# Performance work log

Measured on AMD Instinct MI355X. Metric: run time of the kernel, lower is better.

The kernel has to match this reference:

```python
import jax, jax.numpy as jnp
import numpy as np

N_NODES = 100000
N_EDGES = 800000
IN_DIM = 7
HID = 64
HEADS1 = 4
NUM_CLUSTERS = 4
NEG_SLOPE = 0.2


def setup_inputs() -> dict:
    key = jax.random.key(0)
    ks = jax.random.split(key, 24)
    s = 0.1
    inp = {
        "x": jax.random.uniform(ks[0], (N_NODES, IN_DIM), dtype=jnp.float32),
        "edge_index": jax.random.randint(ks[1], (2, N_EDGES), 0, N_NODES, dtype=jnp.int32),
        "edge_attr": jax.random.normal(ks[2], (N_EDGES, 1), dtype=jnp.float32),
        "assignments": jax.random.randint(ks[3], (N_NODES,), 0, NUM_CLUSTERS, dtype=jnp.int32),
        "W1": jax.random.normal(ks[4], (IN_DIM, HEADS1 * HID), dtype=jnp.float32) * s,
        "att_src1": jax.random.normal(ks[5], (HEADS1, HID), dtype=jnp.float32) * s,
        "att_dst1": jax.random.normal(ks[6], (HEADS1, HID), dtype=jnp.float32) * s,
        "We1": jax.random.normal(ks[7], (1, HEADS1 * HID), dtype=jnp.float32) * s,
        "att_e1": jax.random.normal(ks[8], (HEADS1, HID), dtype=jnp.float32) * s,
        "b1": jnp.zeros((HEADS1 * HID,), dtype=jnp.float32),
        "W2": jax.random.normal(ks[9], (HEADS1 * HID, HID), dtype=jnp.float32) * s,
        "att_src2": jax.random.normal(ks[10], (1, HID), dtype=jnp.float32) * s,
        "att_dst2": jax.random.normal(ks[11], (1, HID), dtype=jnp.float32) * s,
        "We2": jax.random.normal(ks[12], (1, HID), dtype=jnp.float32) * s,
        "att_e2": jax.random.normal(ks[13], (1, HID), dtype=jnp.float32) * s,
        "b2": jnp.zeros((HID,), dtype=jnp.float32),
        # actor MLP: (HID+1) -> HID -> 1
        "A1": jax.random.normal(ks[14], (HID + 1, HID), dtype=jnp.float32) * s,
        "ba1": jnp.zeros((HID,), dtype=jnp.float32),
        "A2": jax.random.normal(ks[15], (HID, 1), dtype=jnp.float32) * s,
        "ba2": jnp.zeros((1,), dtype=jnp.float32),
        # critic MLP: HID*num_clusters -> HID -> 1
        "C1": jax.random.normal(ks[16], (HID * NUM_CLUSTERS, HID), dtype=jnp.float32) * s,
        "bc1": jnp.zeros((HID,), dtype=jnp.float32),
        "C2": jax.random.normal(ks[17], (HID, 1), dtype=jnp.float32) * s,
        "bc2": jnp.zeros((1,), dtype=jnp.float32),
    }
    return inp


def _segment_softmax(logits, seg, n):
    # logits: [E, H]; softmax over edges sharing the same dst node.
    m = jax.ops.segment_max(logits, seg, num_segments=n)
    e = jnp.exp(logits - m[seg])
    z = jax.ops.segment_sum(e, seg, num_segments=n)
    return e / z[seg]


def _gat_conv(x, edge_index, edge_attr, W, att_src, att_dst, We, att_e, bias,
              heads, out_dim, concat, n):
    src, dst = edge_index[0], edge_index[1]
    xh = (x @ W).reshape(n, heads, out_dim)                   # [N,H,D]
    a_src = (xh * att_src[None]).sum(-1)                      # [N,H]
    a_dst = (xh * att_dst[None]).sum(-1)                      # [N,H]
    eh = (edge_attr @ We).reshape(-1, heads, out_dim)         # [E,H,D]
    a_e = (eh * att_e[None]).sum(-1)                          # [E,H]
    alpha = jax.nn.leaky_relu(a_src[src] + a_dst[dst] + a_e, NEG_SLOPE)
    alpha = _segment_softmax(alpha, dst, n)                   # [E,H]
    msg = xh[src] * alpha[:, :, None]                         # [E,H,D]
    out = jax.ops.segment_sum(msg, dst, num_segments=n)       # [N,H,D]
    out = out.reshape(n, heads * out_dim) if concat else out.mean(axis=1)
    return out + bias


def reference(x, edge_index, edge_attr, assignments,
              W1, att_src1, att_dst1, We1, att_e1, b1,
              W2, att_src2, att_dst2, We2, att_e2, b2,
              A1, ba1, A2, ba2, C1, bc1, C2, bc2):
    n = x.shape[0]
    h = jax.nn.elu(_gat_conv(x, edge_index, edge_attr,
                             W1, att_src1, att_dst1, We1, att_e1, b1,
                             HEADS1, HID, True, n))
    h = _gat_conv(h, edge_index, edge_attr,
                  W2, att_src2, att_dst2, We2, att_e2, b2,
                  1, HID, False, n)                            # [N,HID]
    # cluster mean pooling (fused segment-reduce, replaces python loop)
    seg = assignments
    counts = jax.ops.segment_sum(jnp.ones((n,), dtype=h.dtype), seg,
                                 num_segments=NUM_CLUSTERS)
    denom = jnp.maximum(counts, 1.0)[:, None]
    z_clusters = jax.ops.segment_sum(h, seg, num_segments=NUM_CLUSTERS) / denom
    z_clusters = jnp.where(counts[:, None] > 0, z_clusters, 0.0)  # [C,HID]
    cf = jax.ops.segment_sum(x[:, 6], seg, num_segments=NUM_CLUSTERS) / denom[:, 0]
    cf = jnp.where(counts > 0, cf, 0.0)[:, None]                  # [C,1]
    z_with_cf = jnp.concatenate([z_clusters, cf], axis=-1)        # [C,HID+1]
    logits = (jax.nn.relu(z_with_cf @ A1 + ba1) @ A2 + ba2)[:, 0]  # [C]
    z_flat = z_clusters.reshape(1, -1)                             # [1,C*HID]
    value = jax.nn.relu(z_flat @ C1 + bc1) @ C2 + bc2              # [1,1]
    probs = jax.nn.softmax(logits)[None, :]                        # [1,C]
    return probs, value, z_flat
```

## Files before the change

kernel.cpp:

```cpp
#include <hip/hip_runtime.h>
#include <hip/hip_fp16.h>

#define NN 100000
#define NE 800000
#define NZB2 1563
#define NRA 25
#define SRCMASK 0x01FFFFFF

typedef short bf16x8 __attribute__((ext_vector_type(8)));
typedef float f32x4 __attribute__((ext_vector_type(4)));

__device__ __forceinline__ float wave_reduce_sum(float v) {
    #pragma unroll
    for (int o = 32; o > 0; o >>= 1) v += __shfl_down(v, o, 64);
    return v;
}

__device__ __forceinline__ unsigned short f2bf(float f) {
    unsigned u = __float_as_uint(f);
    unsigned r = (u + 0x7FFFu + ((u >> 16) & 1u)) >> 16;
    return (unsigned short)r;
}
__device__ __forceinline__ float bf2f(unsigned short b) {
    return __uint_as_float(((unsigned)b) << 16);
}
__device__ __forceinline__ float bflo(unsigned u) {
    return __uint_as_float(u << 16);
}
__device__ __forceinline__ float bfhi(unsigned u) {
    return __uint_as_float(u & 0xFFFF0000u);
}
__device__ __forceinline__ unsigned pk2(float a, float b) {
    return (unsigned)f2bf(a) | ((unsigned)f2bf(b) << 16);
}
__device__ __forceinline__ unsigned char f2fp8(float f) {
    __half h = __float2half(f * 0.00390625f);
    unsigned short b = __half_as_ushort(h);
    unsigned s = (b >> 8) & 0x80u;
    unsigned mag = b & 0x7FFFu;
    mag = (mag + 0x3Fu + ((mag >> 7) & 1u)) >> 7;
    if (mag > 0x7Eu) mag = 0x7Eu;
    return (unsigned char)(s | mag);
}
__device__ __forceinline__ float dfp8(unsigned v) {
    unsigned short hb = (unsigned short)(((v & 0x80u) << 8) | ((v & 0x7Fu) << 7));
    return __half2float(__ushort_as_half(hb)) * 256.f;
}

__global__ void k_zero(int4* __restrict__ hist4) {
    int i = blockIdx.x * 256 + threadIdx.x;
    if (i < NN / 4) hist4[i] = make_int4(0, 0, 0, 0);
}

__global__ void k_pre(const float* __restrict__ W1, const float* __restrict__ as1,
                      const float* __restrict__ ad1,
                      const float* __restrict__ We1, const float* __restrict__ ae1,
                      const float* __restrict__ We2, const float* __restrict__ ae2,
                      const float* __restrict__ W2, const float* __restrict__ as2,
                      const float* __restrict__ ad2,
                      float* __restrict__ cb, unsigned short* __restrict__ W2fr) {
    int t = threadIdx.x;
    if (blockIdx.x == 0) {
        if (t < 28) {
            int k = t >> 2, h = t & 3;
            float s = 0.f, d = 0.f;
            for (int c = 0; c < 64; ++c) {
                float w = W1[k * 256 + h * 64 + c];
                s += w * as1[h * 64 + c];
                d += w * ad1[h * 64 + c];
            }
            cb[t] = s; cb[28 + t] = d;
        } else if (t < 32) {
            int h = t - 28;
            float s = 0.f;
            for (int c = 0; c < 64; ++c) s += We1[h * 64 + c] * ae1[h * 64 + c];
            cb[56 + h] = s;
        } else if (t == 32) {
            float s = 0.f;
            for (int c = 0; c < 64; ++c) s += We2[c] * ae2[c];
            cb[60] = s;
        }
    } else {
        int o = (blockIdx.x - 1) * 256 + t;
        if (o >= 20480) return;
        int i = o & 7, l = (o >> 3) & 63, rest = o >> 9;
        int ct = rest % 5, ks = rest / 5;
        int k = ks * 32 + ((l >> 4) * 8) + i;
        int cl = l & 15;
        if (ct < 4) {
            W2fr[o] = f2bf(W2[k * 64 + ct * 16 + cl]);
        } else if (cl < 2) {
            const float* av = (cl == 0) ? as2 : ad2;
            float s = 0.f;
            for (int j = 0; j < 64; ++j) s += W2[k * 64 + j] * av[j];
            W2fr[o] = f2bf(s);
        } else {
            W2fr[o] = 0;
        }
    }
}

__global__ void k_node1h(const float* __restrict__ x, const float* __restrict__ cb,
                         const int* __restrict__ dst,
                         uint4* __restrict__ anode, uint4* __restrict__ xpack,
                         int* __restrict__ hist, int* __restrict__ rank) {
    int n = blockIdx.x * 256 + threadIdx.x;
    if (n >= NN) return;
    float xv[7];
    #pragma unroll
    for (int k = 0; k < 7; ++k) xv[k] = x[n * 7 + k];
    float s[4] = {0.f, 0.f, 0.f, 0.f}, d[4] = {0.f, 0.f, 0.f, 0.f};
    #pragma unroll
    for (int k = 0; k < 7; ++k)
        #pragma unroll
        for (int h = 0; h < 4; ++h) {
            s[h] += xv[k] * cb[k * 4 + h];
            d[h] += xv[k] * cb[28 + k * 4 + h];
        }
    anode[n] = make_uint4(pk2(s[0], s[1]), pk2(s[2], s[3]), pk2(d[0], d[1]), pk2(d[2], d[3]));
    xpack[n] = make_uint4(pk2(xv[0], xv[1]), pk2(xv[2], xv[3]),
                          pk2(xv[4], xv[5]), pk2(xv[6], 1.f));
    int e0 = n * 8;
    int4 d0 = *(const int4*)(dst + e0);
    int4 d1 = *(const int4*)(dst + e0 + 4);
    int4 r0, r1;
    r0.x = atomicAdd(&hist[d0.x], 1); r0.y = atomicAdd(&hist[d0.y], 1);
    r0.z = atomicAdd(&hist[d0.z], 1); r0.w = atomicAdd(&hist[d0.w], 1);
    r1.x = atomicAdd(&hist[d1.x], 1); r1.y = atomicAdd(&hist[d1.y], 1);
    r1.z = atomicAdd(&hist[d1.z], 1); r1.w = atomicAdd(&hist[d1.w], 1);
    *(int4*)(rank + e0) = r0;
    *(int4*)(rank + e0 + 4) = r1;
}

__global__ __launch_bounds__(1024) void k_scanA(const int* __restrict__ hist,
                                                int* __restrict__ bsum) {
    __shared__ int ws[16];
    int i = blockIdx.x * 1024 + threadIdx.x;
    int lane = threadIdx.x & 63, wid = threadIdx.x >> 6;
    int v = (i < NN) ? hist[i] : 0;
    #pragma unroll
    for (int o = 32; o; o >>= 1) v += __shfl_down(v, o, 64);
    if (lane == 0) ws[wid] = v;
    __syncthreads();
    if (wid == 0) {
        int u = (lane < 16) ? ws[lane] : 0;
        #pragma unroll
        for (int o = 8; o; o >>= 1) u += __shfl_down(u, o, 64);
        if (lane == 0) bsum[blockIdx.x] = u;
    }
}

__global__ void k_scanB(const int* __restrict__ bsum, int* __restrict__ bexcl) {
    __shared__ int w0tot;
    int t = threadIdx.x, lane = t & 63, wid = t >> 6;
    int v = (t < 98) ? bsum[t] : 0;
    int s = v;
    #pragma unroll
    for (int d = 1; d < 64; d <<= 1) { int u = __shfl_up(s, d, 64); if (lane >= d) s += u; }
    if (t == 63) w0tot = s;
    __syncthreads();
    if (wid == 1) s += w0tot;
    if (t < 98) bexcl[t] = s - v;
}

__global__ __launch_bounds__(1024) void k_scanC(const int* __restrict__ hist,
                                                const int* __restrict__ bexcl,
                                                int* __restrict__ offs) {
    __shared__ int ws[16];
    int b = blockIdx.x;
    int i = b * 1024 + threadIdx.x;
    int lane = threadIdx.x & 63, wid = threadIdx.x >> 6;
    int v = (i < NN) ? hist[i] : 0;
    int s = v;
    #pragma unroll
    for (int d = 1; d < 64; d <<= 1) { int u = __shfl_up(s, d, 64); if (lane >= d) s += u; }
    if (lane == 63) ws[wid] = s;
    __syncthreads();
    if (wid == 0) {
        int u2 = (lane < 16) ? ws[lane] : 0;
        #pragma unroll
        for (int d = 1; d < 16; d <<= 1) { int uu = __shfl_up(u2, d, 64); if (lane >= d) u2 += uu; }
        if (lane < 16) ws[lane] = u2;
    }
    __syncthreads();
    int incl = s + (wid ? ws[wid - 1] : 0) + bexcl[b];
    if (i < NN) offs[i + 1] = incl;
    if (i == 0) offs[0] = 0;
}

__global__ void k_scatter(const int* __restrict__ src, const int* __restrict__ dst,
                          const float* __restrict__ ea, const int* __restrict__ rank,
                          const int* __restrict__ offs,
                          const uint4* __restrict__ anode, const float* __restrict__ cb,
                          int4* __restrict__ es2) {
    int e0 = (blockIdx.x * 256 + threadIdx.x) * 2;
    if (e0 >= NE) return;
    int2 s2 = *(const int2*)(src + e0);
    int2 d2 = *(const int2*)(dst + e0);
    float2 a2 = *(const float2*)(ea + e0);
    int2 r2 = *(const int2*)(rank + e0);
    float c56 = cb[56], c57 = cb[57], c58 = cb[58], c59 = cb[59];
    #pragma unroll
    for (int u = 0; u < 2; ++u) {
        int s = u ? s2.y : s2.x;
        int d = u ? d2.y : d2.x;
        float eav = u ? a2.y : a2.x;
        int pos = offs[d] + (u ? r2.y : r2.x);
        uint4 ar = anode[s];
        uint4 br = anode[d];
        float lg0 = bflo(ar.x) + bflo(br.z) + eav * c56;
        float lg1 = bfhi(ar.x) + bfhi(br.z) + eav * c57;
        float lg2 = bflo(ar.y) + bflo(br.w) + eav * c58;
        float lg3 = bfhi(ar.y) + bfhi(br.w) + eav * c59;
        lg0 = lg0 >= 0.f ? lg0 : 0.2f * lg0;
        lg1 = lg1 >= 0.f ? lg1 : 0.2f * lg1;
        lg2 = lg2 >= 0.f ? lg2 : 0.2f * lg2;
        lg3 = lg3 >= 0.f ? lg3 : 0.2f * lg3;
        unsigned w01 = pk2(__expf(lg0), __expf(lg1));
        unsigned w23 = pk2(__expf(lg2), __expf(lg3));
        es2[pos] = make_int4((int)w01, (int)w23, s | ((d & 63) << 25), __float_as_int(eav));
    }
}

__global__ __launch_bounds__(256, 7) void k_conv1red(
    const uint4* __restrict__ xpack, const float* __restrict__ W1, const float* __restrict__ b1,
    const int* __restrict__ offs, const int4* __restrict__ es2,
    const unsigned short* __restrict__ W2fr,
    unsigned char* __restrict__ xh2f, float* __restrict__ a_src2, float* __restrict__ a_dst2) {
    __shared__ __attribute__((aligned(16))) unsigned char smem[16896];
    uint4* xs = (uint4*)smem;
    uint2* wsx = (uint2*)(smem + 4096);
    typedef unsigned short hsrow[264];
    hsrow* hs = (hsrow*)smem;
    __shared__ int soffs[33];
    __shared__ float ms[32][33];
    int t = threadIdx.x, lane = t & 63, wid = t >> 6;
    int n0 = blockIdx.x * 32;
    if (t <= 32) soffs[t] = offs[n0 + t];
    float w1r[7][4], b1r[4];
    #pragma unroll
    for (int k = 0; k < 7; ++k)
        #pragma unroll
        for (int h = 0; h < 4; ++h) w1r[k][h] = W1[k * 256 + h * 64 + lane];
    #pragma unroll
    for (int h = 0; h < 4; ++h) b1r[h] = b1[h * 64 + lane];
    __syncthreads();
    int E0 = soffs[0], E1 = soffs[32];
    int g = t >> 3, q = t & 7;
    int go0 = soffs[g], go1 = soffs[g + 1];
    int qh = q >> 1;
    int xsl = (q & 1) ? 0 : 16;
    float mh0 = 0.f, mh1 = 0.f, mh2 = 0.f, mh3 = 0.f;
    for (int C0 = E0; C0 < E1; C0 += 256) {
        int C1 = min(C0 + 256, E1);
        int j = C0 + t;
        if (j < C1) {
            int4 e4 = es2[j];
            xs[t] = xpack[e4.z & SRCMASK];
            wsx[t] = make_uint2((unsigned)e4.x, (unsigned)e4.y);
        }
        __syncthreads();
        int lo = max(go0, C0) - C0, hi = min(go1, C1) - C0;
        for (int jj = lo; jj < hi; ++jj) {
            unsigned xu = ((const unsigned*)&xs[jj])[qh];
            float xv = __uint_as_float((xu << xsl) & 0xFFFF0000u);
            uint2 wv = wsx[jj];
            mh0 = fmaf(bflo(wv.x), xv, mh0);
            mh1 = fmaf(bfhi(wv.x), xv, mh1);
            mh2 = fmaf(bflo(wv.y), xv, mh2);
            mh3 = fmaf(bfhi(wv.y), xv, mh3);
        }
        __syncthreads();
    }
    ms[g][0 * 8 + q] = mh0; ms[g][1 * 8 + q] = mh1;
    ms[g][2 * 8 + q] = mh2; ms[g][3 * 8 + q] = mh3;
    __syncthreads();
    for (int gi = wid * 8; gi < wid * 8 + 8; ++gi) {
        bool has = soffs[gi + 1] > soffs[gi];
        #pragma unroll
        for (int h = 0; h < 4; ++h) {
            float rz = __builtin_amdgcn_rcpf(ms[gi][h * 8 + 7]);
            float a = 0.f;
            #pragma unroll
            for (int k = 0; k < 7; ++k) a = fmaf(ms[gi][h * 8 + k], w1r[k][h], a);
            float mm = (has ? a * rz : 0.f) + b1r[h];
            float hv = mm > 0.f ? mm : (__expf(mm) - 1.f);
            hs[gi][h * 64 + lane] = f2bf(hv);
        }
    }
    __syncthreads();
    int row = lane & 15, kg = lane >> 4;
    #pragma unroll
    for (int u = wid; u < 10; u += 4) {
        int nt = u & 1, ct = u >> 1;
        f32x4 acc = {0.f, 0.f, 0.f, 0.f};
        #pragma unroll
        for (int ks = 0; ks < 8; ++ks) {
            bf16x8 av = *(const bf16x8*)&hs[nt * 16 + row][ks * 32 + kg * 8];
            bf16x8 bv = *(const bf16x8*)(W2fr + (((ks * 5 + ct) * 64) + lane) * 8);
            acc = __builtin_amdgcn_mfma_f32_16x16x32_bf16(av, bv, acc, 0, 0, 0);
        }
        if (ct < 4) {
            #pragma unroll
            for (int i = 0; i < 4; ++i)
                xh2f[(n0 + nt * 16 + kg * 4 + i) * 64 + ct * 16 + row] = f2fp8(acc[i]);
        } else if (row == 0) {
            #pragma unroll
            for (int i = 0; i < 4; ++i) a_src2[n0 + nt * 16 + kg * 4 + i] = acc[i];
        } else if (row == 1) {
            #pragma unroll
            for (int i = 0; i < 4; ++i) a_dst2[n0 + nt * 16 + kg * 4 + i] = acc[i];
        }
    }
}

__global__ __launch_bounds__(256) void k_zpool(
    const int4* __restrict__ es2, const int* __restrict__ offs,
    const float* __restrict__ a_src2, const float* __restrict__ a_dst2,
    const int* __restrict__ assign, const float* __restrict__ cb,
    const unsigned char* __restrict__ xh2f, const float* __restrict__ x,
    float* __restrict__ partial) {
    __shared__ int soffs[65];
    __shared__ float adL[64];
    __shared__ int asgL[64];
    __shared__ float ewL[1024];
    __shared__ int sL[1024];
    __shared__ float rzL[64];
    __shared__ float zacc[64];
    __shared__ float csum[264];
    int t = threadIdx.x;
    int n0 = blockIdx.x * 64;
    if (t <= 64) soffs[t] = offs[min(n0 + t, NN)];
    if (t < 64) {
        int nn = min(n0 + t, NN - 1);
        adL[t] = a_dst2[nn];
        asgL[t] = assign[nn];
        zacc[t] = 0.f;
    }
    for (int i = t; i < 264; i += 256) csum[i] = 0.f;
    __syncthreads();
    int E0 = soffs[0], E1 = soffs[64];
    int span = E1 - E0;
    float c2 = cb[60];
    #pragma unroll
    for (int c0 = 0; c0 < 1024; c0 += 256) {
        int j = c0 + t;
        if (j < span && j < 1024) {
            int4 e4 = es2[E0 + j];
            int sx = e4.z & SRCMASK;
            int d6 = (e4.z >> 25) & 63;
            float lg = a_src2[sx] + adL[d6] + __int_as_float(e4.w) * c2;
            lg = lg >= 0.f ? lg : 0.2f * lg;
            ewL[j] = __expf(lg);
            sL[j] = e4.z;
        }
    }
    for (int j = 1024 + t; j < span; j += 256) {
        int4 e4 = es2[E0 + j];
        int d6 = (e4.z >> 25) & 63;
        float lg = a_src2[e4.z & SRCMASK] + adL[d6] + __int_as_float(e4.w) * c2;
        lg = lg >= 0.f ? lg : 0.2f * lg;
        atomicAdd(&zacc[d6], __expf(lg));
    }
    __syncthreads();
    int gz = t >> 2, q4 = t & 3;
    {
        int lo = soffs[gz] - E0, hi = soffs[gz + 1] - E0;
        int hicap = min(hi, 1024);
        float z = 0.f;
        for (int jj = lo + q4; jj < hicap; jj += 4) z += ewL[jj];
        z += __shfl_xor(z, 1, 64);
        z += __shfl_xor(z, 2, 64);
        if (q4 == 0) rzL[gz] = __builtin_amdgcn_rcpf(z + zacc[gz]);
    }
    __syncthreads();
    int slot = t >> 3, q = t & 7;
    const unsigned char* pbase = xh2f + q * 8;
    float ac[4][8];
    #pragma unroll
    for (int c = 0; c < 4; ++c)
        #pragma unroll
        for (int k = 0; k < 8; ++k) ac[c][k] = 0.f;
    #pragma unroll 2
    for (int jj = slot; jj < span; jj += 32) {
        int zv; float ew;
        if (jj < 1024) {
            zv = sL[jj];
            ew = ewL[jj];
        } else {
            int4 e4 = es2[E0 + jj];
            zv = e4.z;
            int d6o = (zv >> 25) & 63;
            float lg = a_src2[zv & SRCMASK] + adL[d6o] + __int_as_float(e4.w) * c2;
            lg = lg >= 0.f ? lg : 0.2f * lg;
            ew = __expf(lg);
        }
        int sx = zv & SRCMASK;
        int d6 = (zv >> 25) & 63;
        float wv = ew * rzL[d6];
        int cc = asgL[d6];
        uint2 u = *(const uint2*)(pbase + sx * 64);
        float v0 = dfp8(u.x & 255u), v1 = dfp8((u.x >> 8) & 255u);
        float v2 = dfp8((u.x >> 16) & 255u), v3 = dfp8(u.x >> 24);
        float v4 = dfp8(u.y & 255u), v5 = dfp8((u.y >> 8) & 255u);
        float v6 = dfp8((u.y >> 16) & 255u), v7 = dfp8(u.y >> 24);
        #pragma unroll
        for (int c = 0; c < 4; ++c) {
            float wc = (cc == c) ? wv : 0.f;
            ac[c][0] = fmaf(wc, v0, ac[c][0]);
            ac[c][1] = fmaf(wc, v1, ac[c][1]);
            ac[c][2] = fmaf(wc, v2, ac[c][2]);
            ac[c][3] = fmaf(wc, v3, ac[c][3]);
            ac[c][4] = fmaf(wc, v4, ac[c][4]);
            ac[c][5] = fmaf(wc, v5, ac[c][5]);
            ac[c][6] = fmaf(wc, v6, ac[c][6]);
            ac[c][7] = fmaf(wc, v7, ac[c][7]);
        }
    }
    #pragma unroll
    for (int c = 0; c < 4; ++c)
        #pragma unroll
        for (int k = 0; k < 8; ++k) {
            float v = ac[c][k];
            v += __shfl_xor(v, 8, 64);
            v += __shfl_xor(v, 16, 64);
            v += __shfl_xor(v, 32, 64);
            ac[c][k] = v;
        }
    if (((t >> 3) & 7) == 0) {
        #pragma unroll
        for (int c = 0; c < 4; ++c)
            #pragma unroll
            for (int k = 0; k < 8; ++k)
                atomicAdd(&csum[c * 64 + q * 8 + k], ac[c][k]);
    }
    if (t < 64 && n0 + t < NN) {
        int c = asgL[t];
        atomicAdd(&csum[256 + c], 1.f);
        atomicAdd(&csum[260 + c], x[(n0 + t) * 7 + 6]);
    }
    __syncthreads();
    for (int i = t; i < 264; i += 256) partial[blockIdx.x * 264 + i] = csum[i];
}

__global__ __launch_bounds__(256) void k_redA(const float* __restrict__ partial,
                                              float* __restrict__ part2) {
    int gblk = blockIdx.x;
    int b0 = gblk * 64, b1 = min(b0 + 64, NZB2);
    int t = threadIdx.x;
    for (int i = t; i < 264; i += 256) {
        float s = 0.f;
        for (int b = b0; b < b1; ++b) s += partial[b * 264 + i];
        part2[gblk * 264 + i] = s;
    }
}

__global__ __launch_bounds__(256) void k_redB(const float* __restrict__ part2,
                                              float* __restrict__ gacc) {
    int t = threadIdx.x;
    for (int i = t; i < 264; i += 256) {
        float s = 0.f;
        for (int g = 0; g < NRA; ++g) s += part2[g * 264 + i];
        gacc[i] = s;
    }
}

__global__ __launch_bounds__(256) void k_head(
    const float* __restrict__ gacc, const float* __restrict__ b2,
    const float* __restrict__ A1, const float* __restrict__ ba1,
    const float* __restrict__ A2, const float* __restrict__ ba2,
    const float* __restrict__ C1, const float* __restrict__ bc1,
    const float* __restrict__ C2, const float* __restrict__ bc2,
    float* __restrict__ out) {
    __shared__ float zc[4][64];
    __shared__ float cfs[4];
    __shared__ float logits[4];
    __shared__ float vpart[4][64];
    int t = threadIdx.x;
    int j = t & 63, wv = t >> 6;
    float cnt = gacc[256 + wv];
    float den = fmaxf(cnt, 1.f);
    zc[wv][j] = (cnt > 0.f) ? (gacc[wv * 64 + j] + cnt * b2[j]) / den : 0.f;
    if (t < 4) {
        float cc = gacc[256 + t];
        cfs[t] = (cc > 0.f) ? gacc[260 + t] / fmaxf(cc, 1.f) : 0.f;
    }
    __syncthreads();
    float tv = ba1[j];
    for (int k = 0; k < 64; ++k) tv = fmaf(zc[wv][k], A1[k * 64 + j], tv);
    tv = fmaf(cfs[wv], A1[64 * 64 + j], tv);
    tv = fmaxf(tv, 0.f);
    float sred = wave_reduce_sum(tv * A2[j]);
    if (j == 0) logits[wv] = sred + ba2[0];
    float vj = (wv == 0) ? bc1[j] : 0.f;
    for (int kk = 0; kk < 64; ++kk) vj = fmaf(zc[wv][kk], C1[(wv * 64 + kk) * 64 + j], vj);
    vpart[wv][j] = vj;
    __syncthreads();
    if (wv == 0) {
        float vv = fmaxf(vpart[0][j] + vpart[1][j] + vpart[2][j] + vpart[3][j], 0.f);
        float v = wave_reduce_sum(vv * C2[j]);
        if (j == 0) {
            float m = fmaxf(fmaxf(logits[0], logits[1]), fmaxf(logits[2], logits[3]));
            float e0 = __expf(logits[0] - m), e1 = __expf(logits[1] - m);
            float e2 = __expf(logits[2] - m), e3 = __expf(logits[3] - m);
            float sum = e0 + e1 + e2 + e3;
            out[0] = e0 / sum; out[1] = e1 / sum; out[2] = e2 / sum; out[3] = e3 / sum;
            out[4] = v + bc2[0];
        }
    }
    out[5 + wv * 64 + j] = zc[wv][j];
}

extern "C" void kernel_launch(void* const* d_in, const int* in_sizes, int n_in,
                              void* d_out, int out_size, void* d_ws, size_t ws_size,
                              hipStream_t stream) {
    const float* x    = (const float*)d_in[0];
    const int*   ei   = (const int*)d_in[1];
    const float* ea   = (const float*)d_in[2];
    const int*   asg  = (const int*)d_in[3];
    const float* W1   = (const float*)d_in[4];
    const float* as1  = (const float*)d_in[5];
    const float* ad1  = (const float*)d_in[6];
    const float* We1  = (const float*)d_in[7];
    const float* ae1  = (const float*)d_in[8];
    const float* b1   = (const float*)d_in[9];
    const float* W2   = (const float*)d_in[10];
    const float* as2  = (const float*)d_in[11];
    const float* ad2  = (const float*)d_in[12];
    const float* We2  = (const float*)d_in[13];
    const float* ae2  = (const float*)d_in[14];
    const float* b2   = (const float*)d_in[15];
    const float* A1   = (const float*)d_in[16];
    const float* ba1  = (const float*)d_in[17];
    const float* A2   = (const float*)d_in[18];
    const float* ba2  = (const float*)d_in[19];
    const float* C1   = (const float*)d_in[20];
    const float* bc1  = (const float*)d_in[21];
    const float* C2   = (const float*)d_in[22];
    const float* bc2  = (const float*)d_in[23];
    const int* src = ei;
    const int* dst = ei + NE;

    char* w = (char*)d_ws;
    size_t off = 0;
    auto alloc = [&](size_t bytes) -> void* {
        void* p = w + off;
        off += (bytes + 255) & ~(size_t)255;
        return p;
    };
    int*   hist   = (int*)alloc(NN * sizeof(int));
    float* gacc   = (float*)alloc(264 * sizeof(float));
    float* partial= (float*)alloc((size_t)NZB2 * 264 * sizeof(float));
    float* part2  = (float*)alloc((size_t)NRA * 264 * sizeof(float));
    uint4* anode  = (uint4*)alloc(NN * sizeof(uint4));
    float* a_src2 = (float*)alloc(NN * sizeof(float));
    float* a_dst2 = (float*)alloc(NN * sizeof(float));
    uint4* xpack  = (uint4*)alloc(NN * sizeof(uint4));
    int*   offs   = (int*)alloc((NN + 1) * sizeof(int));
    int*   rank   = (int*)alloc(NE * sizeof(int));
    int*   bsum   = (int*)alloc(128 * sizeof(int));
    int*   bexcl  = (int*)alloc(128 * sizeof(int));
    int4*  es2    = (int4*)alloc(NE * sizeof(int4));
    unsigned char* xh2f = (unsigned char*)alloc((size_t)NN * 64 * sizeof(unsigned char));
    unsigned short* W2fr = (unsigned short*)alloc(20480 * sizeof(unsigned short));
    float* cb     = (float*)alloc(64 * sizeof(float));
    (void)ws_size; (void)n_in; (void)in_sizes; (void)out_size;

    k_zero<<<98, 256, 0, stream>>>((int4*)hist);
    k_pre<<<81, 256, 0, stream>>>(W1, as1, ad1, We1, ae1, We2, ae2, W2, as2, ad2, cb, W2fr);
    k_node1h<<<(NN + 255) / 256, 256, 0, stream>>>(x, cb, dst, anode, xpack, hist, rank);
    k_scanA<<<98, 1024, 0, stream>>>(hist, bsum);
    k_scanB<<<1, 128, 0, stream>>>(bsum, bexcl);
    k_scanC<<<98, 1024, 0, stream>>>(hist, bexcl, offs);
    k_scatter<<<(NE / 2 + 255) / 256, 256, 0, stream>>>(src, dst, ea, rank, offs,
                                                        anode, cb, es2);
    k_conv1red<<<NN / 32, 256, 0, stream>>>(xpack, W1, b1, offs, es2,
                                            W2fr, xh2f, a_src2, a_dst2);
    k_zpool<<<NZB2, 256, 0, stream>>>(es2, offs, a_src2, a_dst2, asg, cb, xh2f, x, partial);
    k_redA<<<NRA, 256, 0, stream>>>(partial, part2);
    k_redB<<<1, 256, 0, stream>>>(part2, gacc);
    k_head<<<1, 256, 0, stream>>>(gacc, b2, A1, ba1, A2, ba2, C1, bc1, C2, bc2, (float*)d_out);
}
```

Before: 174.7 us.

## Move conv1 edge-weight computation from scatter into conv1 reduction, shrink edge records

The conv1 attention logits and exp are now computed in the conv1 reduction kernel instead of the CSR scatter kernel. The per-edge record drops from 16 to 8 bytes, holding only the packed src/dst-low bits and the edge attribute. The per-node attention scalars and packed x are interleaved into one 32-byte record, so a single source gather brings in both. This cuts random gathers and write traffic in the scatter kernel and halves edge-record reads in the pooling kernel. In exchange the reduction kernel does more per-edge math, and it indexes the destination by the low 5 bits, which relies on 32-node blocks aligned to 32.

```diff
diff --git a/kernel.cpp b/kernel.cpp
--- a/kernel.cpp
+++ b/kernel.cpp
@@ -102,8 +102,8 @@
 
 __global__ void k_node1h(const float* __restrict__ x, const float* __restrict__ cb,
                          const int* __restrict__ dst,
-                         uint4* __restrict__ anode, uint4* __restrict__ xpack,
-                         int* __restrict__ hist, int* __restrict__ rank) {
+                         uint4* __restrict__ nrec, int* __restrict__ hist,
+                         int* __restrict__ rank) {
     int n = blockIdx.x * 256 + threadIdx.x;
     if (n >= NN) return;
     float xv[7];
@@ -117,9 +117,10 @@
             s[h] += xv[k] * cb[k * 4 + h];
             d[h] += xv[k] * cb[28 + k * 4 + h];
         }
-    anode[n] = make_uint4(pk2(s[0], s[1]), pk2(s[2], s[3]), pk2(d[0], d[1]), pk2(d[2], d[3]));
-    xpack[n] = make_uint4(pk2(xv[0], xv[1]), pk2(xv[2], xv[3]),
-                          pk2(xv[4], xv[5]), pk2(xv[6], 1.f));
+    nrec[2 * n] = make_uint4(pk2(s[0], s[1]), pk2(s[2], s[3]),
+                             pk2(d[0], d[1]), pk2(d[2], d[3]));
+    nrec[2 * n + 1] = make_uint4(pk2(xv[0], xv[1]), pk2(xv[2], xv[3]),
+                                 pk2(xv[4], xv[5]), pk2(xv[6], 1.f));
     int e0 = n * 8;
     int4 d0 = *(const int4*)(dst + e0);
     int4 d1 = *(const int4*)(dst + e0 + 4);
@@ -190,42 +191,23 @@
 
 __global__ void k_scatter(const int* __restrict__ src, const int* __restrict__ dst,
                           const float* __restrict__ ea, const int* __restrict__ rank,
-                          const int* __restrict__ offs,
-                          const uint4* __restrict__ anode, const float* __restrict__ cb,
-                          int4* __restrict__ es2) {
+                          const int* __restrict__ offs, int2* __restrict__ es2) {
     int e0 = (blockIdx.x * 256 + threadIdx.x) * 2;
     if (e0 >= NE) return;
     int2 s2 = *(const int2*)(src + e0);
     int2 d2 = *(const int2*)(dst + e0);
     float2 a2 = *(const float2*)(ea + e0);
     int2 r2 = *(const int2*)(rank + e0);
-    float c56 = cb[56], c57 = cb[57], c58 = cb[58], c59 = cb[59];
-    #pragma unroll
-    for (int u = 0; u < 2; ++u) {
-        int s = u ? s2.y : s2.x;
-        int d = u ? d2.y : d2.x;
-        float eav = u ? a2.y : a2.x;
-        int pos = offs[d] + (u ? r2.y : r2.x);
-        uint4 ar = anode[s];
-        uint4 br = anode[d];
-        float lg0 = bflo(ar.x) + bflo(br.z) + eav * c56;
-        float lg1 = bfhi(ar.x) + bfhi(br.z) + eav * c57;
-        float lg2 = bflo(ar.y) + bflo(br.w) + eav * c58;
-        float lg3 = bfhi(ar.y) + bfhi(br.w) + eav * c59;
-        lg0 = lg0 >= 0.f ? lg0 : 0.2f * lg0;
-        lg1 = lg1 >= 0.f ? lg1 : 0.2f * lg1;
-        lg2 = lg2 >= 0.f ? lg2 : 0.2f * lg2;
-        lg3 = lg3 >= 0.f ? lg3 : 0.2f * lg3;
-        unsigned w01 = pk2(__expf(lg0), __expf(lg1));
-        unsigned w23 = pk2(__expf(lg2), __expf(lg3));
-        es2[pos] = make_int4((int)w01, (int)w23, s | ((d & 63) << 25), __float_as_int(eav));
-    }
+    int p0 = offs[d2.x] + r2.x;
+    int p1 = offs[d2.y] + r2.y;
+    es2[p0] = make_int2(s2.x | ((d2.x & 63) << 25), __float_as_int(a2.x));
+    es2[p1] = make_int2(s2.y | ((d2.y & 63) << 25), __float_as_int(a2.y));
 }
 
 __global__ __launch_bounds__(256, 7) void k_conv1red(
-    const uint4* __restrict__ xpack, const float* __restrict__ W1, const float* __restrict__ b1,
-    const int* __restrict__ offs, const int4* __restrict__ es2,
-    const unsigned short* __restrict__ W2fr,
+    const uint4* __restrict__ nrec, const float* __restrict__ W1, const float* __restrict__ b1,
+    const float* __restrict__ cb, const int* __restrict__ offs,
+    const int2* __restrict__ es2, const unsigned short* __restrict__ W2fr,
     unsigned char* __restrict__ xh2f, float* __restrict__ a_src2, float* __restrict__ a_dst2) {
     __shared__ __attribute__((aligned(16))) unsigned char smem[16896];
     uint4* xs = (uint4*)smem;
@@ -233,10 +215,15 @@
     typedef unsigned short hsrow[264];
     hsrow* hs = (hsrow*)smem;
     __shared__ int soffs[33];
+    __shared__ uint2 ad1L[32];
     __shared__ float ms[32][33];
     int t = threadIdx.x, lane = t & 63, wid = t >> 6;
     int n0 = blockIdx.x * 32;
     if (t <= 32) soffs[t] = offs[n0 + t];
+    if (t < 32) {
+        uint4 a = nrec[2 * (n0 + t)];
+        ad1L[t] = make_uint2(a.z, a.w);
+    }
     float w1r[7][4], b1r[4];
     #pragma unroll
     for (int k = 0; k < 7; ++k)
@@ -244,6 +231,7 @@
         for (int h = 0; h < 4; ++h) w1r[k][h] = W1[k * 256 + h * 64 + lane];
     #pragma unroll
     for (int h = 0; h < 4; ++h) b1r[h] = b1[h * 64 + lane];
+    float c56 = cb[56], c57 = cb[57], c58 = cb[58], c59 = cb[59];
     __syncthreads();
     int E0 = soffs[0], E1 = soffs[32];
     int g = t >> 3, q = t & 7;
@@ -255,9 +243,23 @@
         int C1 = min(C0 + 256, E1);
         int j = C0 + t;
         if (j < C1) {
-            int4 e4 = es2[j];
-            xs[t] = xpack[e4.z & SRCMASK];
-            wsx[t] = make_uint2((unsigned)e4.x, (unsigned)e4.y);
+            int2 e2 = es2[j];
+            int sx = e2.x & SRCMASK;
+            int dl = (e2.x >> 25) & 31;
+            float eav = __int_as_float(e2.y);
+            uint4 ar = nrec[2 * sx];
+            xs[t] = nrec[2 * sx + 1];
+            uint2 br = ad1L[dl];
+            float lg0 = bflo(ar.x) + bflo(br.x) + eav * c56;
+            float lg1 = bfhi(ar.x) + bfhi(br.x) + eav * c57;
+            float lg2 = bflo(ar.y) + bflo(br.y) + eav * c58;
+            float lg3 = bfhi(ar.y) + bfhi(br.y) + eav * c59;
+            lg0 = lg0 >= 0.f ? lg0 : 0.2f * lg0;
+            lg1 = lg1 >= 0.f ? lg1 : 0.2f * lg1;
+            lg2 = lg2 >= 0.f ? lg2 : 0.2f * lg2;
+            lg3 = lg3 >= 0.f ? lg3 : 0.2f * lg3;
+            wsx[t] = make_uint2(pk2(__expf(lg0), __expf(lg1)),
+                                pk2(__expf(lg2), __expf(lg3)));
         }
         __syncthreads();
         int lo = max(go0, C0) - C0, hi = min(go1, C1) - C0;
@@ -315,7 +317,7 @@
 }
 
 __global__ __launch_bounds__(256) void k_zpool(
-    const int4* __restrict__ es2, const int* __restrict__ offs,
+    const int2* __restrict__ es2, const int* __restrict__ offs,
     const float* __restrict__ a_src2, const float* __restrict__ a_dst2,
     const int* __restrict__ assign, const float* __restrict__ cb,
     const unsigned char* __restrict__ xh2f, const float* __restrict__ x,
@@ -346,19 +348,19 @@
     for (int c0 = 0; c0 < 1024; c0 += 256) {
         int j = c0 + t;
         if (j < span && j < 1024) {
-            int4 e4 = es2[E0 + j];
-            int sx = e4.z & SRCMASK;
-            int d6 = (e4.z >> 25) & 63;
-            float lg = a_src2[sx] + adL[d6] + __int_as_float(e4.w) * c2;
+            int2 e2 = es2[E0 + j];
+            int sx = e2.x & SRCMASK;
+            int d6 = (e2.x >> 25) & 63;
+            float lg = a_src2[sx] + adL[d6] + __int_as_float(e2.y) * c2;
             lg = lg >= 0.f ? lg : 0.2f * lg;
             ewL[j] = __expf(lg);
-            sL[j] = e4.z;
+            sL[j] = e2.x;
         }
     }
     for (int j = 1024 + t; j < span; j += 256) {
-        int4 e4 = es2[E0 + j];
-        int d6 = (e4.z >> 25) & 63;
-        float lg = a_src2[e4.z & SRCMASK] + adL[d6] + __int_as_float(e4.w) * c2;
+        int2 e2 = es2[E0 + j];
+        int d6 = (e2.x >> 25) & 63;
+        float lg = a_src2[e2.x & SRCMASK] + adL[d6] + __int_as_float(e2.y) * c2;
         lg = lg >= 0.f ? lg : 0.2f * lg;
         atomicAdd(&zacc[d6], __expf(lg));
     }
@@ -388,10 +390,10 @@
             zv = sL[jj];
             ew = ewL[jj];
         } else {
-            int4 e4 = es2[E0 + jj];
-            zv = e4.z;
+            int2 e2 = es2[E0 + jj];
+            zv = e2.x;
             int d6o = (zv >> 25) & 63;
-            float lg = a_src2[zv & SRCMASK] + adL[d6o] + __int_as_float(e4.w) * c2;
+            float lg = a_src2[zv & SRCMASK] + adL[d6o] + __int_as_float(e2.y) * c2;
             lg = lg >= 0.f ? lg : 0.2f * lg;
             ew = __expf(lg);
         }
@@ -552,15 +554,14 @@
     float* gacc   = (float*)alloc(264 * sizeof(float));
     float* partial= (float*)alloc((size_t)NZB2 * 264 * sizeof(float));
     float* part2  = (float*)alloc((size_t)NRA * 264 * sizeof(float));
-    uint4* anode  = (uint4*)alloc(NN * sizeof(uint4));
+    uint4* nrec   = (uint4*)alloc((size_t)NN * 2 * sizeof(uint4));
     float* a_src2 = (float*)alloc(NN * sizeof(float));
     float* a_dst2 = (float*)alloc(NN * sizeof(float));
-    uint4* xpack  = (uint4*)alloc(NN * sizeof(uint4));
     int*   offs   = (int*)alloc((NN + 1) * sizeof(int));
     int*   rank   = (int*)alloc(NE * sizeof(int));
     int*   bsum   = (int*)alloc(128 * sizeof(int));
     int*   bexcl  = (int*)alloc(128 * sizeof(int));
-    int4*  es2    = (int4*)alloc(NE * sizeof(int4));
+    int2*  es2    = (int2*)alloc(NE * sizeof(int2));
     unsigned char* xh2f = (unsigned char*)alloc((size_t)NN * 64 * sizeof(unsigned char));
     unsigned short* W2fr = (unsigned short*)alloc(20480 * sizeof(unsigned short));
     float* cb     = (float*)alloc(64 * sizeof(float));
@@ -568,13 +569,12 @@
 
     k_zero<<<98, 256, 0, stream>>>((int4*)hist);
     k_pre<<<81, 256, 0, stream>>>(W1, as1, ad1, We1, ae1, We2, ae2, W2, as2, ad2, cb, W2fr);
-    k_node1h<<<(NN + 255) / 256, 256, 0, stream>>>(x, cb, dst, anode, xpack, hist, rank);
+    k_node1h<<<(NN + 255) / 256, 256, 0, stream>>>(x, cb, dst, nrec, hist, rank);
     k_scanA<<<98, 1024, 0, stream>>>(hist, bsum);
     k_scanB<<<1, 128, 0, stream>>>(bsum, bexcl);
     k_scanC<<<98, 1024, 0, stream>>>(hist, bexcl, offs);
-    k_scatter<<<(NE / 2 + 255) / 256, 256, 0, stream>>>(src, dst, ea, rank, offs,
-                                                        anode, cb, es2);
-    k_conv1red<<<NN / 32, 256, 0, stream>>>(xpack, W1, b1, offs, es2,
+    k_scatter<<<(NE / 2 + 255) / 256, 256, 0, stream>>>(src, dst, ea, rank, offs, es2);
+    k_conv1red<<<NN / 32, 256, 0, stream>>>(nrec, W1, b1, cb, offs, es2,
                                             W2fr, xh2f, a_src2, a_dst2);
     k_zpool<<<NZB2, 256, 0, stream>>>(es2, offs, a_src2, a_dst2, asg, cb, xh2f, x, partial);
     k_redA<<<NRA, 256, 0, stream>>>(partial, part2);
```

After: 168.9 us. -3.3%, faster.
